# Performance work log

Hardware: AMD Instinct MI355X
Metric: run time of the kernel (lower is better)

## Reference

```python
import jax, jax.numpy as jnp
import numpy as np

NUM_HEADS = 4

def setup_inputs() -> dict:
    key = jax.random.key(0)
    ks = jax.random.split(key, 5)
    B, H, W, C = 4, 64, 64, 256
    x = jax.random.normal(ks[0], (B, H, W, C), dtype=jnp.float32)
    w_qkv = jax.random.normal(ks[1], (C, 3 * C), dtype=jnp.float32) * (C ** -0.5)
    b_qkv = jax.random.normal(ks[2], (3 * C,), dtype=jnp.float32) * 0.02
    w_out = jax.random.normal(ks[3], (C, C), dtype=jnp.float32) * (C ** -0.5)
    b_out = jax.random.normal(ks[4], (C,), dtype=jnp.float32) * 0.02
    return {"x": x, "w_qkv": w_qkv, "b_qkv": b_qkv, "w_out": w_out, "b_out": b_out}

def reference(x, w_qkv, b_qkv, w_out, b_out):
    B, H, W, C = x.shape
    nh = NUM_HEADS
    hd = C // nh
    scale = hd ** -0.5
    N = H * W
    # qkv projection: [B, N, 3, nh, hd]
    qkv = (x.reshape(B, N, C) @ w_qkv + b_qkv).reshape(B, N, 3, nh, hd)
    q, k, v = jnp.moveaxis(qkv, 2, 0)          # each [B, N, nh, hd]
    q = jnp.swapaxes(q, 1, 2)                  # [B, nh, N, hd]
    k = jnp.swapaxes(k, 1, 2)
    v = jnp.swapaxes(v, 1, 2)
    attn = jax.nn.softmax(jnp.einsum('bhnd,bhmd->bhnm', q * scale, k), axis=-1)
    o = jnp.einsum('bhnm,bhmd->bhnd', attn, v)  # [B, nh, N, hd]
    o = jnp.swapaxes(o, 1, 2).reshape(B, H, W, C)
    return o @ w_out + b_out
```

## Files before the change

### kernel.cpp

```cpp
#include <hip/hip_runtime.h>
#include <stdint.h>

typedef unsigned short u16;
typedef __attribute__((ext_vector_type(8))) short bf16x8;
typedef __attribute__((ext_vector_type(4))) float f32x4;

#define QSCL 0.1803368801111244f

#define GLD_LDS16(g, l) __builtin_amdgcn_global_load_lds( \
    (const __attribute__((address_space(1))) void*)(g),    \
    (__attribute__((address_space(3))) void*)(l), 16, 0, 0)

#if __has_builtin(__builtin_amdgcn_exp2f)
#define EXP2(x) __builtin_amdgcn_exp2f(x)
#else
#define EXP2(x) __builtin_exp2f(x)
#endif

__device__ __forceinline__ u16 f2bf(float f) {
    union { uint32_t i; float f; } v; v.f = f;
    uint32_t i = v.i;
    return (u16)((i + 0x7FFFu + ((i >> 16) & 1u)) >> 16);
}

__global__ __launch_bounds__(256)
void transpose_kernel(const float* __restrict__ src, u16* __restrict__ dst,
                      int R, int Ctiles) {
    __shared__ u16 T[64][68];
    const int t = threadIdx.x;
    const int rt = blockIdx.x / Ctiles;
    const int ct = blockIdx.x % Ctiles;
    const int C = Ctiles << 6;

    for (int i = 0; i < 4; i++) {
        int idx = t + 256 * i;
        int row = idx >> 4;
        int col4 = (idx & 15) << 2;
        float4 d = *(const float4*)(src + (size_t)(rt * 64 + row) * C + ct * 64 + col4);
        T[col4 + 0][row] = f2bf(d.x);
        T[col4 + 1][row] = f2bf(d.y);
        T[col4 + 2][row] = f2bf(d.z);
        T[col4 + 3][row] = f2bf(d.w);
    }
    __syncthreads();
    for (int i = 0; i < 4; i++) {
        int idx = t + 256 * i;
        int row = idx >> 4;
        int col4 = (idx & 15) << 2;
        uint2 d = *(const uint2*)&T[row][col4];
        *(uint2*)(dst + (size_t)(ct * 64 + row) * R + rt * 64 + col4) = d;
    }
}

__global__ __launch_bounds__(256)
void convert_kernel(const float* __restrict__ x, u16* __restrict__ xbf) {
    size_t i = ((size_t)blockIdx.x * 256 + threadIdx.x) * 4;
    float4 d = *(const float4*)(x + i);
    u16 e[4] = {f2bf(d.x), f2bf(d.y), f2bf(d.z), f2bf(d.w)};
    *(uint2*)(xbf + i) = *(uint2*)e;
}

__global__ __launch_bounds__(256)
void gemm_qkv_old(const float* __restrict__ X, const u16* __restrict__ Wt,
                  const float* __restrict__ Bias, u16* __restrict__ QK,
                  u16* __restrict__ Vt) {
    __shared__ __align__(16) u16 As[64][40];
    __shared__ __align__(16) u16 Bts[64][40];

    const int t = threadIdx.x;
    const int lane = t & 63;
    const int wave = t >> 6;
    const int l15 = lane & 15;
    const int l4 = lane >> 4;

    const int ntile = blockIdx.x % 12;
    const int mbase = (blockIdx.x / 12) << 6;

    f32x4 acc[4];
    for (int c = 0; c < 4; c++) acc[c] = (f32x4){0.f, 0.f, 0.f, 0.f};

    for (int kc = 0; kc < 256; kc += 32) {
        __syncthreads();
        for (int i = 0; i < 2; i++) {
            int idx = t + 256 * i;
            int row = idx >> 3;
            int col4 = (idx & 7) << 2;
            float4 d = *(const float4*)(X + (size_t)(mbase + row) * 256 + kc + col4);
            u16 e[4] = {f2bf(d.x), f2bf(d.y), f2bf(d.z), f2bf(d.w)};
            *(uint2*)&As[row][col4] = *(uint2*)e;
        }
        for (int i = 0; i < 2; i++) {
            int idx = t + 256 * i;
            int row = idx >> 3;
            int col4 = (idx & 7) << 2;
            uint2 w = *(const uint2*)(Wt + (size_t)(ntile * 64 + row) * 256 + kc + col4);
            *(uint2*)&Bts[row][col4] = w;
        }
        __syncthreads();

        bf16x8 a = *(const bf16x8*)&As[wave * 16 + l15][l4 * 8];
        for (int c = 0; c < 4; c++) {
            bf16x8 b = *(const bf16x8*)&Bts[c * 16 + l15][l4 * 8];
            acc[c] = __builtin_amdgcn_mfma_f32_16x16x32_bf16(a, b, acc[c], 0, 0, 0);
        }
    }

    if (ntile < 8) {
        const float scl = (ntile < 4) ? QSCL : 1.0f;
        for (int c = 0; c < 4; c++) {
            int colc = c * 16 + l15;
            float bv = Bias[ntile * 64 + colc];
            for (int r = 0; r < 4; r++) {
                int row = mbase + wave * 16 + l4 * 4 + r;
                QK[(size_t)row * 512 + ntile * 64 + colc] = f2bf((acc[c][r] + bv) * scl);
            }
        }
    } else {
        const int h = ntile - 8;
        for (int c = 0; c < 4; c++) {
            int d = c * 16 + l15;
            float bv = Bias[512 + h * 64 + d];
            int n = mbase + wave * 16 + l4 * 4;
            int b = n >> 12;
            int nin = n & 4095;
            u16 e[4] = {f2bf(acc[c][0] + bv), f2bf(acc[c][1] + bv),
                        f2bf(acc[c][2] + bv), f2bf(acc[c][3] + bv)};
            *(uint2*)(Vt + ((size_t)(b * 4 + h) * 64 + d) * 4096 + nin) = *(uint2*)e;
        }
    }
}

__global__ __launch_bounds__(256)
void gemm_out_old(const u16* __restrict__ Wt2, const float* __restrict__ Bias,
                  float* __restrict__ IO) {
    __shared__ __align__(16) u16 As[64][264];
    __shared__ __align__(16) u16 Wts[256][40];

    const int t = threadIdx.x;
    const int lane = t & 63;
    const int wave = t >> 6;
    const int l15 = lane & 15;
    const int l4 = lane >> 4;
    const int mbase = blockIdx.x << 6;

    for (int i = 0; i < 16; i++) {
        int idx = t + 256 * i;
        int row = idx >> 6;
        int col4 = (idx & 63) << 2;
        float4 d = *(const float4*)(IO + (size_t)(mbase + row) * 256 + col4);
        u16 e[4] = {f2bf(d.x), f2bf(d.y), f2bf(d.z), f2bf(d.w)};
        *(uint2*)&As[row][col4] = *(uint2*)e;
    }

    f32x4 acc[4][4];
    for (int nt = 0; nt < 4; nt++)
        for (int c = 0; c < 4; c++) acc[nt][c] = (f32x4){0.f, 0.f, 0.f, 0.f};

    for (int kc = 0; kc < 256; kc += 32) {
        __syncthreads();
        for (int i = 0; i < 8; i++) {
            int idx = t + 256 * i;
            int row = idx >> 3;
            int col4 = (idx & 7) << 2;
            uint2 w = *(const uint2*)(Wt2 + (size_t)row * 256 + kc + col4);
            *(uint2*)&Wts[row][col4] = w;
        }
        __syncthreads();

        bf16x8 a = *(const bf16x8*)&As[wave * 16 + l15][kc + l4 * 8];
        for (int nt = 0; nt < 4; nt++)
            for (int c = 0; c < 4; c++) {
                bf16x8 b = *(const bf16x8*)&Wts[nt * 64 + c * 16 + l15][l4 * 8];
                acc[nt][c] = __builtin_amdgcn_mfma_f32_16x16x32_bf16(a, b, acc[nt][c], 0, 0, 0);
            }
    }

    for (int nt = 0; nt < 4; nt++)
        for (int c = 0; c < 4; c++) {
            int coln = nt * 64 + c * 16 + l15;
            float bv = Bias[coln];
            for (int r = 0; r < 4; r++) {
                int row = mbase + wave * 16 + l4 * 4 + r;
                IO[(size_t)row * 256 + coln] = acc[nt][c][r] + bv;
            }
        }
}

__global__ __launch_bounds__(256)
void gemm_qkv_new(const u16* __restrict__ Abf, const u16* __restrict__ Bt,
                  const float* __restrict__ Bias, u16* __restrict__ QK,
                  u16* __restrict__ Vt) {
    __shared__ __align__(16) u16 As[128 * 32];
    __shared__ __align__(16) u16 Bs[128 * 32];

    const int t = threadIdx.x;
    const int lane = t & 63;
    const int wave = t >> 6;
    const int l15 = lane & 15;
    const int l4 = lane >> 4;
    const int wm = wave >> 1, wn = wave & 1;

    const int mb = blockIdx.x / 6;
    const int nb = blockIdx.x % 6;

    const u16* gA[2]; const u16* gB[2]; int ldsoff[2];
    #pragma unroll
    for (int i = 0; i < 2; i++) {
        int chunk = i * 256 + t;
        int row = chunk >> 2;
        int sch = (chunk & 3) ^ (row & 3);
        gA[i] = Abf + (size_t)(mb * 128 + row) * 256 + sch * 8;
        gB[i] = Bt + (size_t)(nb * 128 + row) * 256 + sch * 8;
        ldsoff[i] = (i * 256 + wave * 64) * 8;
    }
    int offA[4], offB[4];
    #pragma unroll
    for (int c = 0; c < 4; c++) {
        offA[c] = (wm * 64 + c * 16 + l15) * 32 + ((l4 ^ (l15 & 3)) * 8);
        offB[c] = (wn * 64 + c * 16 + l15) * 32 + ((l4 ^ (l15 & 3)) * 8);
    }

    f32x4 acc[4][4];
    #pragma unroll
    for (int cm = 0; cm < 4; cm++)
        for (int cn = 0; cn < 4; cn++) acc[cm][cn] = (f32x4){0.f, 0.f, 0.f, 0.f};

    for (int kc = 0; kc < 256; kc += 32) {
        __syncthreads();
        #pragma unroll
        for (int i = 0; i < 2; i++) {
            GLD_LDS16(gA[i] + kc, As + ldsoff[i]);
            GLD_LDS16(gB[i] + kc, Bs + ldsoff[i]);
        }
        __syncthreads();

        bf16x8 a[4], b[4];
        #pragma unroll
        for (int c = 0; c < 4; c++) {
            a[c] = *(const bf16x8*)(As + offA[c]);
            b[c] = *(const bf16x8*)(Bs + offB[c]);
        }
        #pragma unroll
        for (int cm = 0; cm < 4; cm++)
            #pragma unroll
            for (int cn = 0; cn < 4; cn++)
                acc[cm][cn] = __builtin_amdgcn_mfma_f32_16x16x32_bf16(
                    a[cm], b[cn], acc[cm][cn], 0, 0, 0);
    }

    #pragma unroll
    for (int cn = 0; cn < 4; cn++) {
        int n = nb * 128 + wn * 64 + cn * 16 + l15;
        float bv = Bias[n];
        int slice = n >> 6;
        if (slice < 4) {
            #pragma unroll
            for (int cm = 0; cm < 4; cm++) {
                int m0 = mb * 128 + wm * 64 + cm * 16 + l4 * 4;
                for (int r = 0; r < 4; r++)
                    QK[(size_t)(m0 + r) * 512 + n] = f2bf((acc[cm][cn][r] + bv) * QSCL);
            }
        } else if (slice < 8) {
            #pragma unroll
            for (int cm = 0; cm < 4; cm++) {
                int m0 = mb * 128 + wm * 64 + cm * 16 + l4 * 4;
                for (int r = 0; r < 4; r++)
                    QK[(size_t)(m0 + r) * 512 + n] = f2bf(acc[cm][cn][r] + bv);
            }
        } else {
            int h = slice - 8;
            int d = n & 63;
            #pragma unroll
            for (int cm = 0; cm < 4; cm++) {
                int m0 = mb * 128 + wm * 64 + cm * 16 + l4 * 4;
                int b_ = m0 >> 12;
                int nin = m0 & 4095;
                u16 e[4] = {f2bf(acc[cm][cn][0] + bv), f2bf(acc[cm][cn][1] + bv),
                            f2bf(acc[cm][cn][2] + bv), f2bf(acc[cm][cn][3] + bv)};
                *(uint2*)(Vt + ((size_t)(b_ * 4 + h) * 64 + d) * 4096 + nin) = *(uint2*)e;
            }
        }
    }
}

__global__ __launch_bounds__(256)
void gemm_out_new(const u16* __restrict__ Obf, const u16* __restrict__ Wt2,
                  const float* __restrict__ Bias, float* __restrict__ out) {
    __shared__ __align__(16) u16 As[128 * 32];
    __shared__ __align__(16) u16 Bs[128 * 32];

    const int t = threadIdx.x;
    const int lane = t & 63;
    const int wave = t >> 6;
    const int l15 = lane & 15;
    const int l4 = lane >> 4;
    const int wm = wave >> 1, wn = wave & 1;

    const int mb = blockIdx.x >> 1;
    const int nb = blockIdx.x & 1;

    const u16* gA[2]; const u16* gB[2]; int ldsoff[2];
    #pragma unroll
    for (int i = 0; i < 2; i++) {
        int chunk = i * 256 + t;
        int row = chunk >> 2;
        int sch = (chunk & 3) ^ (row & 3);
        gA[i] = Obf + (size_t)(mb * 128 + row) * 256 + sch * 8;
        gB[i] = Wt2 + (size_t)(nb * 128 + row) * 256 + sch * 8;
        ldsoff[i] = (i * 256 + wave * 64) * 8;
    }
    int offA[4], offB[4];
    #pragma unroll
    for (int c = 0; c < 4; c++) {
        offA[c] = (wm * 64 + c * 16 + l15) * 32 + ((l4 ^ (l15 & 3)) * 8);
        offB[c] = (wn * 64 + c * 16 + l15) * 32 + ((l4 ^ (l15 & 3)) * 8);
    }

    f32x4 acc[4][4];
    #pragma unroll
    for (int cm = 0; cm < 4; cm++)
        for (int cn = 0; cn < 4; cn++) acc[cm][cn] = (f32x4){0.f, 0.f, 0.f, 0.f};

    for (int kc = 0; kc < 256; kc += 32) {
        __syncthreads();
        #pragma unroll
        for (int i = 0; i < 2; i++) {
            GLD_LDS16(gA[i] + kc, As + ldsoff[i]);
            GLD_LDS16(gB[i] + kc, Bs + ldsoff[i]);
        }
        __syncthreads();

        bf16x8 a[4], b[4];
        #pragma unroll
        for (int c = 0; c < 4; c++) {
            a[c] = *(const bf16x8*)(As + offA[c]);
            b[c] = *(const bf16x8*)(Bs + offB[c]);
        }
        #pragma unroll
        for (int cm = 0; cm < 4; cm++)
            #pragma unroll
            for (int cn = 0; cn < 4; cn++)
                acc[cm][cn] = __builtin_amdgcn_mfma_f32_16x16x32_bf16(
                    a[cm], b[cn], acc[cm][cn], 0, 0, 0);
    }

    #pragma unroll
    for (int cn = 0; cn < 4; cn++) {
        int n = nb * 128 + wn * 64 + cn * 16 + l15;
        float bv = Bias[n];
        #pragma unroll
        for (int cm = 0; cm < 4; cm++) {
            int m0 = mb * 128 + wm * 64 + cm * 16 + l4 * 4;
            for (int r = 0; r < 4; r++)
                out[(size_t)(m0 + r) * 256 + n] = acc[cm][cn][r] + bv;
        }
    }
}

__global__ __launch_bounds__(256, 4)
void attn_kernel(const u16* __restrict__ QK, const u16* __restrict__ Vt,
                 float* __restrict__ Of, u16* __restrict__ Obf, int writebf,
                 int bhmask, int bhbits) {
    __shared__ __align__(16) u16 Kt[2][64][64];
    __shared__ __align__(16) u16 Vts[2][64][64];
    __shared__ __align__(16) u16 Ps[4][16][64];

    const int t = threadIdx.x;
    const int lane = t & 63;
    const int wave = t >> 6;
    const int l15 = lane & 15;
    const int l4 = lane >> 4;

    const int bh = blockIdx.x & bhmask;
    const int qb = blockIdx.x >> bhbits;
    const int b = bh >> 2;
    const int h = bh & 3;

    const size_t qkbase = (size_t)b * 4096 * 512;
    const size_t vtbase = (size_t)bh * 64 * 4096;
    const int q0 = qb * 64 + wave * 16;

    const u16* gk[2]; const u16* gv[2]; u16* lk[2]; u16* lv[2];
    #pragma unroll
    for (int i = 0; i < 2; i++) {
        int chunk = i * 256 + t;
        int row = chunk >> 3;
        int sch = (chunk & 7) ^ ((row ^ (row >> 3)) & 7);
        gk[i] = QK + qkbase + (size_t)row * 512 + 256 + h * 64 + sch * 8;
        gv[i] = Vt + vtbase + (size_t)row * 4096 + sch * 8;
        int cbase = (i * 256 + wave * 64) * 8;
        lk[i] = &Kt[0][0][0] + cbase;
        lv[i] = &Vts[0][0][0] + cbase;
    }
    int koff[4][2];
    #pragma unroll
    for (int c = 0; c < 4; c++) {
        int row = c * 16 + l15;
        int sw = (row ^ (row >> 3)) & 7;
        koff[c][0] = row * 64 + ((0 + l4) ^ sw) * 8;
        koff[c][1] = row * 64 + ((4 + l4) ^ sw) * 8;
    }
    u16* psbase = &Ps[wave][l15][0];
    int offw[4], offr[2];
    #pragma unroll
    for (int c = 0; c < 4; c++)
        offw[c] = (((2 * c + (l4 >> 1)) ^ (l15 & 7)) << 3) + ((l4 & 1) << 2);
    #pragma unroll
    for (int kk = 0; kk < 2; kk++)
        offr[kk] = (((4 * kk + l4) ^ (l15 & 7)) << 3);

    bf16x8 qf[2];
    #pragma unroll
    for (int kk = 0; kk < 2; kk++)
        qf[kk] = *(const bf16x8*)(QK + qkbase
            + (size_t)(q0 + l15) * 512 + h * 64 + kk * 32 + l4 * 8);

    const f32x4 z4 = (f32x4){0.f, 0.f, 0.f, 0.f};

    f32x4 Oacc[4];
    #pragma unroll
    for (int c = 0; c < 4; c++) Oacc[c] = z4;
    float lsum = 0.f;

    auto stageKV = [&](int buf, int jn) {
        #pragma unroll
        for (int i = 0; i < 2; i++) {
            GLD_LDS16(gk[i] + (size_t)jn * 32768, lk[i] + buf * 4096);
            GLD_LDS16(gv[i] + jn * 64,            lv[i] + buf * 4096);
        }
    };

    auto body = [&](int par, int jn) {
        __syncthreads();
        stageKV(par ^ 1, jn);

        const u16* kb = &Kt[0][0][0] + par * 4096;
        const u16* vb = &Vts[0][0][0] + par * 4096;

        f32x4 s[4];
        #pragma unroll
        for (int c = 0; c < 4; c++) {
            bf16x8 k0 = *(const bf16x8*)(kb + koff[c][0]);
            bf16x8 k1 = *(const bf16x8*)(kb + koff[c][1]);
            s[c] = __builtin_amdgcn_mfma_f32_16x16x32_bf16(k0, qf[0], z4, 0, 0, 0);
            s[c] = __builtin_amdgcn_mfma_f32_16x16x32_bf16(k1, qf[1], s[c], 0, 0, 0);
        }

        float ls = 0.f;
        #pragma unroll
        for (int c = 0; c < 4; c++) {
            f32x4 sv = s[c];
            float p0 = EXP2(sv[0]);
            float p1 = EXP2(sv[1]);
            float p2 = EXP2(sv[2]);
            float p3 = EXP2(sv[3]);
            ls += (p0 + p1) + (p2 + p3);
            uint2 pk;
            asm("v_cvt_pk_bf16_f32 %0, %1, %2" : "=v"(pk.x) : "v"(p0), "v"(p1));
            asm("v_cvt_pk_bf16_f32 %0, %1, %2" : "=v"(pk.y) : "v"(p2), "v"(p3));
            *(uint2*)(psbase + offw[c]) = pk;
        }
        lsum += ls;

        __threadfence_block();

        bf16x8 bp[2];
        #pragma unroll
        for (int kk = 0; kk < 2; kk++)
            bp[kk] = *(const bf16x8*)(psbase + offr[kk]);

        #pragma unroll
        for (int c = 0; c < 4; c++) {
            bf16x8 v0 = *(const bf16x8*)(vb + koff[c][0]);
            bf16x8 v1 = *(const bf16x8*)(vb + koff[c][1]);
            Oacc[c] = __builtin_amdgcn_mfma_f32_16x16x32_bf16(v0, bp[0], Oacc[c], 0, 0, 0);
            Oacc[c] = __builtin_amdgcn_mfma_f32_16x16x32_bf16(v1, bp[1], Oacc[c], 0, 0, 0);
        }
    };

    stageKV(0, 0);
    for (int jt = 0; jt < 64; jt += 2) {
        body(0, jt + 1);
        body(1, (jt + 2) & 63);
    }

    float l = lsum;
    l += __shfl_xor(l, 16);
    l += __shfl_xor(l, 32);
    float inv = 1.f / l;
    size_t row = (size_t)b * 4096 + q0 + l15;
    if (writebf) {
        #pragma unroll
        for (int c = 0; c < 4; c++) {
            f32x4 o = Oacc[c] * inv;
            u16 e[4] = {f2bf(o[0]), f2bf(o[1]), f2bf(o[2]), f2bf(o[3])};
            *(uint2*)(Obf + row * 256 + h * 64 + c * 16 + l4 * 4) = *(uint2*)e;
        }
    } else {
        #pragma unroll
        for (int c = 0; c < 4; c++) {
            f32x4 o = Oacc[c] * inv;
            *(f32x4*)(Of + row * 256 + h * 64 + c * 16 + l4 * 4) = o;
        }
    }
}

extern "C" void kernel_launch(void* const* d_in, const int* in_sizes, int n_in,
                              void* d_out, int out_size, void* d_ws, size_t ws_size,
                              hipStream_t stream) {
    const float* x     = (const float*)d_in[0];
    const float* w_qkv = (const float*)d_in[1];
    const float* b_qkv = (const float*)d_in[2];
    const float* w_out = (const float*)d_in[3];
    const float* b_out = (const float*)d_in[4];
    float* out = (float*)d_out;

    char* ws = (char*)d_ws;
    u16* Wt  = (u16*)ws;
    u16* Wt2 = (u16*)(ws + 393216);
    u16* QK  = (u16*)(ws + 524288);
    u16* Vt  = (u16*)(ws + 524288 + 16777216);
    u16* XO  = (u16*)(ws + 524288 + 16777216 + 8388608);
    const size_t NEED_NEW = 524288 + 16777216 + 8388608 + 8388608;

    transpose_kernel<<<dim3(48), dim3(256), 0, stream>>>(w_qkv, Wt, 256, 12);
    transpose_kernel<<<dim3(16), dim3(256), 0, stream>>>(w_out, Wt2, 256, 4);

    if (ws_size >= NEED_NEW) {
        convert_kernel<<<dim3(4096), dim3(256), 0, stream>>>(x, XO);
        gemm_qkv_new<<<dim3(768), dim3(256), 0, stream>>>(XO, Wt, b_qkv, QK, Vt);
        attn_kernel<<<dim3(1024), dim3(256), 0, stream>>>(
            QK, Vt, out, XO, 1, 15, 4);
        gemm_out_new<<<dim3(256), dim3(256), 0, stream>>>(XO, Wt2, b_out, out);
    } else {
        gemm_qkv_old<<<dim3(3072), dim3(256), 0, stream>>>(x, Wt, b_qkv, QK, Vt);
        attn_kernel<<<dim3(1024), dim3(256), 0, stream>>>(
            QK, Vt, out, (u16*)nullptr, 0, 15, 4);
        gemm_out_old<<<dim3(256), dim3(256), 0, stream>>>(Wt2, b_out, out);
    }
}
```

Before: 213.2 us.

## Switch attention to 32x32x16 MFMA with register-only P via permlane32 swap

The attention inner loop now uses 32x32x16 bf16 MFMAs. Each wave handles 32 queries by 32 keys, with the key dimension split across wave pairs. The P tile is repacked in registers with permlane32_swap instead of a round trip through LDS. This removes the Ps shared buffer and its fence. The two key-halves' partial outputs and row sums are merged through LDS at the end, which costs one extra reduction phase and more accumulator registers.

Measured after the change: 189.1 us. -11.3%, faster.

```diff
diff --git a/kernel.cpp b/kernel.cpp
--- a/kernel.cpp
+++ b/kernel.cpp
@@ -4,6 +4,7 @@
 typedef unsigned short u16;
 typedef __attribute__((ext_vector_type(8))) short bf16x8;
 typedef __attribute__((ext_vector_type(4))) float f32x4;
+typedef __attribute__((ext_vector_type(16))) float f32x16;
 
 #define QSCL 0.1803368801111244f
 
@@ -21,6 +22,26 @@
     union { uint32_t i; float f; } v; v.f = f;
     uint32_t i = v.i;
     return (u16)((i + 0x7FFFu + ((i >> 16) & 1u)) >> 16);
+}
+
+__device__ __forceinline__ void p32swap(uint32_t& a, uint32_t& b) {
+#if __has_builtin(__builtin_amdgcn_permlane32_swap)
+    auto r = __builtin_amdgcn_permlane32_swap(a, b, false, false);
+    a = (uint32_t)r[0]; b = (uint32_t)r[1];
+#else
+    const int hh = (int)((threadIdx.x & 63) >> 5);
+    uint32_t ta = (uint32_t)__shfl_xor((int)a, 32);
+    uint32_t tb = (uint32_t)__shfl_xor((int)b, 32);
+    uint32_t na = hh ? tb : a;
+    uint32_t nb = hh ? b : ta;
+    a = na; b = nb;
+#endif
+}
+
+__device__ __forceinline__ bf16x8 mk8(uint32_t a, uint32_t b, uint32_t c, uint32_t d) {
+    union { uint32_t u[4]; bf16x8 v; } x;
+    x.u[0] = a; x.u[1] = b; x.u[2] = c; x.u[3] = d;
+    return x.v;
 }
 
 __global__ __launch_bounds__(256)
@@ -363,63 +384,64 @@
                  int bhmask, int bhbits) {
     __shared__ __align__(16) u16 Kt[2][64][64];
     __shared__ __align__(16) u16 Vts[2][64][64];
-    __shared__ __align__(16) u16 Ps[4][16][64];
 
     const int t = threadIdx.x;
     const int lane = t & 63;
     const int wave = t >> 6;
-    const int l15 = lane & 15;
-    const int l4 = lane >> 4;
+    const int l31 = lane & 31;
+    const int h = lane >> 5;
+    const int jw = wave & 1;
+    const int qw = wave >> 1;
 
     const int bh = blockIdx.x & bhmask;
     const int qb = blockIdx.x >> bhbits;
     const int b = bh >> 2;
-    const int h = bh & 3;
+    const int hd = bh & 3;
 
     const size_t qkbase = (size_t)b * 4096 * 512;
     const size_t vtbase = (size_t)bh * 64 * 4096;
-    const int q0 = qb * 64 + wave * 16;
+    const int q = qb * 64 + qw * 32 + l31;
 
     const u16* gk[2]; const u16* gv[2]; u16* lk[2]; u16* lv[2];
     #pragma unroll
     for (int i = 0; i < 2; i++) {
-        int chunk = i * 256 + t;
-        int row = chunk >> 3;
-        int sch = (chunk & 7) ^ ((row ^ (row >> 3)) & 7);
-        gk[i] = QK + qkbase + (size_t)row * 512 + 256 + h * 64 + sch * 8;
+        int ck = i * 256 + t;
+        int row = ck >> 3;
+        int sch = (ck & 7) ^ (row & 7);
+        gk[i] = QK + qkbase + (size_t)row * 512 + 256 + hd * 64 + sch * 8;
         gv[i] = Vt + vtbase + (size_t)row * 4096 + sch * 8;
-        int cbase = (i * 256 + wave * 64) * 8;
-        lk[i] = &Kt[0][0][0] + cbase;
-        lv[i] = &Vts[0][0][0] + cbase;
-    }
-    int koff[4][2];
-    #pragma unroll
-    for (int c = 0; c < 4; c++) {
-        int row = c * 16 + l15;
-        int sw = (row ^ (row >> 3)) & 7;
-        koff[c][0] = row * 64 + ((0 + l4) ^ sw) * 8;
-        koff[c][1] = row * 64 + ((4 + l4) ^ sw) * 8;
-    }
-    u16* psbase = &Ps[wave][l15][0];
-    int offw[4], offr[2];
-    #pragma unroll
-    for (int c = 0; c < 4; c++)
-        offw[c] = (((2 * c + (l4 >> 1)) ^ (l15 & 7)) << 3) + ((l4 & 1) << 2);
-    #pragma unroll
-    for (int kk = 0; kk < 2; kk++)
-        offr[kk] = (((4 * kk + l4) ^ (l15 & 7)) << 3);
-
-    bf16x8 qf[2];
-    #pragma unroll
-    for (int kk = 0; kk < 2; kk++)
-        qf[kk] = *(const bf16x8*)(QK + qkbase
-            + (size_t)(q0 + l15) * 512 + h * 64 + kk * 32 + l4 * 8);
-
-    const f32x4 z4 = (f32x4){0.f, 0.f, 0.f, 0.f};
-
-    f32x4 Oacc[4];
-    #pragma unroll
-    for (int c = 0; c < 4; c++) Oacc[c] = z4;
+        lk[i] = &Kt[0][0][0] + (i * 256 + wave * 64) * 8;
+        lv[i] = &Vts[0][0][0] + (i * 256 + wave * 64) * 8;
+    }
+
+    int kfo[4];
+    {
+        int row = jw * 32 + l31;
+        int sw = row & 7;
+        #pragma unroll
+        for (int dc = 0; dc < 4; dc++)
+            kfo[dc] = row * 64 + ((dc * 2 + h) ^ sw) * 8;
+    }
+    int vfo[2][2];
+    #pragma unroll
+    for (int dh = 0; dh < 2; dh++) {
+        int row = dh * 32 + l31;
+        int sw = row & 7;
+        #pragma unroll
+        for (int J = 0; J < 2; J++)
+            vfo[dh][J] = row * 64 + ((jw * 4 + J * 2 + h) ^ sw) * 8;
+    }
+
+    bf16x8 qf[4];
+    #pragma unroll
+    for (int dc = 0; dc < 4; dc++)
+        qf[dc] = *(const bf16x8*)(QK + qkbase + (size_t)q * 512
+                                  + hd * 64 + dc * 16 + h * 8);
+
+    const f32x16 z16 = {0.f, 0.f, 0.f, 0.f, 0.f, 0.f, 0.f, 0.f,
+                        0.f, 0.f, 0.f, 0.f, 0.f, 0.f, 0.f, 0.f};
+    f32x16 Oacc[2];
+    Oacc[0] = z16; Oacc[1] = z16;
     float lsum = 0.f;
 
     auto stageKV = [&](int buf, int jn) {
@@ -437,45 +459,43 @@
         const u16* kb = &Kt[0][0][0] + par * 4096;
         const u16* vb = &Vts[0][0][0] + par * 4096;
 
-        f32x4 s[4];
-        #pragma unroll
-        for (int c = 0; c < 4; c++) {
-            bf16x8 k0 = *(const bf16x8*)(kb + koff[c][0]);
-            bf16x8 k1 = *(const bf16x8*)(kb + koff[c][1]);
-            s[c] = __builtin_amdgcn_mfma_f32_16x16x32_bf16(k0, qf[0], z4, 0, 0, 0);
-            s[c] = __builtin_amdgcn_mfma_f32_16x16x32_bf16(k1, qf[1], s[c], 0, 0, 0);
-        }
-
+        bf16x8 kf0 = *(const bf16x8*)(kb + kfo[0]);
+        bf16x8 kf1 = *(const bf16x8*)(kb + kfo[1]);
+        bf16x8 kf2 = *(const bf16x8*)(kb + kfo[2]);
+        bf16x8 kf3 = *(const bf16x8*)(kb + kfo[3]);
+
+        f32x16 s;
+        s = __builtin_amdgcn_mfma_f32_32x32x16_bf16(kf0, qf[0], z16, 0, 0, 0);
+        s = __builtin_amdgcn_mfma_f32_32x32x16_bf16(kf1, qf[1], s, 0, 0, 0);
+        s = __builtin_amdgcn_mfma_f32_32x32x16_bf16(kf2, qf[2], s, 0, 0, 0);
+        s = __builtin_amdgcn_mfma_f32_32x32x16_bf16(kf3, qf[3], s, 0, 0, 0);
+
+        bf16x8 vf00 = *(const bf16x8*)(vb + vfo[0][0]);
+        bf16x8 vf01 = *(const bf16x8*)(vb + vfo[0][1]);
+        bf16x8 vf10 = *(const bf16x8*)(vb + vfo[1][0]);
+        bf16x8 vf11 = *(const bf16x8*)(vb + vfo[1][1]);
+
+        uint32_t w[8];
         float ls = 0.f;
         #pragma unroll
-        for (int c = 0; c < 4; c++) {
-            f32x4 sv = s[c];
-            float p0 = EXP2(sv[0]);
-            float p1 = EXP2(sv[1]);
-            float p2 = EXP2(sv[2]);
-            float p3 = EXP2(sv[3]);
-            ls += (p0 + p1) + (p2 + p3);
-            uint2 pk;
-            asm("v_cvt_pk_bf16_f32 %0, %1, %2" : "=v"(pk.x) : "v"(p0), "v"(p1));
-            asm("v_cvt_pk_bf16_f32 %0, %1, %2" : "=v"(pk.y) : "v"(p2), "v"(p3));
-            *(uint2*)(psbase + offw[c]) = pk;
+        for (int k = 0; k < 8; k++) {
+            float p0 = EXP2(s[2 * k]);
+            float p1 = EXP2(s[2 * k + 1]);
+            ls += p0 + p1;
+            asm("v_cvt_pk_bf16_f32 %0, %1, %2" : "=v"(w[k]) : "v"(p0), "v"(p1));
         }
         lsum += ls;
 
-        __threadfence_block();
-
-        bf16x8 bp[2];
-        #pragma unroll
-        for (int kk = 0; kk < 2; kk++)
-            bp[kk] = *(const bf16x8*)(psbase + offr[kk]);
-
-        #pragma unroll
-        for (int c = 0; c < 4; c++) {
-            bf16x8 v0 = *(const bf16x8*)(vb + koff[c][0]);
-            bf16x8 v1 = *(const bf16x8*)(vb + koff[c][1]);
-            Oacc[c] = __builtin_amdgcn_mfma_f32_16x16x32_bf16(v0, bp[0], Oacc[c], 0, 0, 0);
-            Oacc[c] = __builtin_amdgcn_mfma_f32_16x16x32_bf16(v1, bp[1], Oacc[c], 0, 0, 0);
-        }
+        p32swap(w[0], w[2]); p32swap(w[1], w[3]);
+        p32swap(w[4], w[6]); p32swap(w[5], w[7]);
+
+        bf16x8 bp0 = mk8(w[0], w[1], w[2], w[3]);
+        bf16x8 bp1 = mk8(w[4], w[5], w[6], w[7]);
+
+        Oacc[0] = __builtin_amdgcn_mfma_f32_32x32x16_bf16(vf00, bp0, Oacc[0], 0, 0, 0);
+        Oacc[0] = __builtin_amdgcn_mfma_f32_32x32x16_bf16(vf01, bp1, Oacc[0], 0, 0, 0);
+        Oacc[1] = __builtin_amdgcn_mfma_f32_32x32x16_bf16(vf10, bp0, Oacc[1], 0, 0, 0);
+        Oacc[1] = __builtin_amdgcn_mfma_f32_32x32x16_bf16(vf11, bp1, Oacc[1], 0, 0, 0);
     };
 
     stageKV(0, 0);
@@ -484,24 +504,50 @@
         body(1, (jt + 2) & 63);
     }
 
-    float l = lsum;
-    l += __shfl_xor(l, 16);
-    l += __shfl_xor(l, 32);
-    float inv = 1.f / l;
-    size_t row = (size_t)b * 4096 + q0 + l15;
-    if (writebf) {
-        #pragma unroll
-        for (int c = 0; c < 4; c++) {
-            f32x4 o = Oacc[c] * inv;
-            u16 e[4] = {f2bf(o[0]), f2bf(o[1]), f2bf(o[2]), f2bf(o[3])};
-            *(uint2*)(Obf + row * 256 + h * 64 + c * 16 + l4 * 4) = *(uint2*)e;
-        }
-    } else {
-        #pragma unroll
-        for (int c = 0; c < 4; c++) {
-            f32x4 o = Oacc[c] * inv;
-            *(f32x4*)(Of + row * 256 + h * 64 + c * 16 + l4 * 4) = o;
-        }
+    lsum += __shfl_xor(lsum, 32);
+
+    __syncthreads();
+    float* sc  = (float*)&Kt[0][0][0];
+    float* scl = (float*)&Vts[0][0][0];
+    const int swl = lane & 7;
+
+    if (jw) {
+        float* ob = sc + qw * 2048 + lane * 32;
+        #pragma unroll
+        for (int dh = 0; dh < 2; dh++)
+            #pragma unroll
+            for (int i = 0; i < 4; i++) {
+                int k8 = dh * 4 + i;
+                f32x4 c = {Oacc[dh][4 * i + 0], Oacc[dh][4 * i + 1],
+                           Oacc[dh][4 * i + 2], Oacc[dh][4 * i + 3]};
+                *(f32x4*)(ob + ((k8 ^ swl) * 4)) = c;
+            }
+        scl[qw * 64 + lane] = lsum;
+    }
+    __syncthreads();
+    if (!jw) {
+        float* ob = sc + qw * 2048 + lane * 32;
+        float lt = lsum + scl[qw * 64 + lane];
+        float inv = 1.f / lt;
+        size_t row = (size_t)b * 4096 + q;
+        #pragma unroll
+        for (int dh = 0; dh < 2; dh++)
+            #pragma unroll
+            for (int i = 0; i < 4; i++) {
+                int k8 = dh * 4 + i;
+                f32x4 pR = *(f32x4*)(ob + ((k8 ^ swl) * 4));
+                f32x4 o;
+                #pragma unroll
+                for (int r = 0; r < 4; r++)
+                    o[r] = (Oacc[dh][4 * i + r] + pR[r]) * inv;
+                int col = hd * 64 + dh * 32 + i * 8 + h * 4;
+                if (writebf) {
+                    u16 e[4] = {f2bf(o[0]), f2bf(o[1]), f2bf(o[2]), f2bf(o[3])};
+                    *(uint2*)(Obf + row * 256 + col) = *(uint2*)e;
+                } else {
+                    *(f32x4*)(Of + row * 256 + col) = o;
+                }
+            }
     }
 }
 
```
